# Optimization experiments

Hardware: AMD Instinct MI355X
Metric: run time of the kernel (lower is better)

The kernel has to match this reference:

```python
import jax, jax.numpy as jnp
import numpy as np

DIM = 128
B = 262144


def setup_inputs() -> dict:
    key = jax.random.key(0)
    k_t, k_w1, k_b1, k_w2, k_b2 = jax.random.split(key, 5)
    t = jax.random.uniform(k_t, (B,), dtype=jnp.float32)  # t in [0, 1]
    s = 1.0 / np.sqrt(DIM)  # torch Linear default init scale
    W1 = jax.random.uniform(k_w1, (DIM, DIM), dtype=jnp.float32, minval=-s, maxval=s)
    b1 = jax.random.uniform(k_b1, (DIM,), dtype=jnp.float32, minval=-s, maxval=s)
    W2 = jax.random.uniform(k_w2, (DIM, DIM), dtype=jnp.float32, minval=-s, maxval=s)
    b2 = jax.random.uniform(k_b2, (DIM,), dtype=jnp.float32, minval=-s, maxval=s)
    return {"t": t, "W1": W1, "b1": b1, "W2": W2, "b2": b2}


def reference(t, W1, b1, W2, b2):
    # create_timestep_embedding, vectorized over batch and dim:
    #   emb[b, i] = t[b]*cos(i/dim*pi*t[b]) + t[b]*sin(i/dim*pi*(1 - t[b]))
    phase = (jnp.arange(DIM, dtype=t.dtype) / DIM) * jnp.pi  # [DIM]
    tb = t[:, None]  # [B, 1]
    emb = tb * jnp.cos(phase[None, :] * tb) + tb * jnp.sin(phase[None, :] * (1.0 - tb))  # [B, DIM]
    x = jax.nn.silu(emb @ W1.T + b1)  # Linear128 + SiLU
    x = jax.nn.silu(x @ W2.T + b2)    # Linear128 + SiLU
    return x
```

## Files before the change

### kernel.cpp

```cpp
#include <hip/hip_runtime.h>

typedef _Float16 f16;
typedef _Float16 f16x2 __attribute__((ext_vector_type(2)));
typedef _Float16 f16x8 __attribute__((ext_vector_type(8)));
typedef float    f32x16 __attribute__((ext_vector_type(16)));

#define DIM 128

__device__ __forceinline__ float silu_f(float x) {
    float e = __builtin_amdgcn_exp2f(x * -1.44269504088896341f);
    return x * __builtin_amdgcn_rcpf(1.0f + e);
}

__global__ __launch_bounds__(512, 2)
void ts_mlp_kernel(const float* __restrict__ t,
                   const float* __restrict__ W1, const float* __restrict__ b1,
                   const float* __restrict__ W2, const float* __restrict__ b2,
                   float* __restrict__ out, int B) {
    __shared__ f16x8 w1f[8][4][64];
    __shared__ f16x8 w2f[8][4][64];
    __shared__ f16x2 x1p[8][512][4];

    const int tid  = threadIdx.x;
    const int wv   = tid >> 6;
    const int lane = tid & 63;
    const int h    = lane >> 5;
    const int l31  = lane & 31;
    const int par  = lane & 1;

    {
        const int kt = wv;
        const int k0 = kt * 16 + h * 8;
#pragma unroll
        for (int mtx = 0; mtx < 2; ++mtx) {
            const float* W = mtx ? W2 : W1;
#pragma unroll
            for (int nt = 0; nt < 4; ++nt) {
                const int n = nt * 32 + l31;
                const float4* src = (const float4*)(W + n * DIM + k0);
                float4 lo = src[0], hi = src[1];
                f16x8 fr;
                fr[0] = (f16)lo.x; fr[1] = (f16)lo.y; fr[2] = (f16)lo.z; fr[3] = (f16)lo.w;
                fr[4] = (f16)hi.x; fr[5] = (f16)hi.y; fr[6] = (f16)hi.z; fr[7] = (f16)hi.w;
                if (mtx) w2f[kt][nt][lane] = fr; else w1f[kt][nt][lane] = fr;
            }
        }
    }
    float b1v[4], b2v[4];
#pragma unroll
    for (int nt = 0; nt < 4; ++nt) {
        b1v[nt] = b1[nt * 32 + l31];
        b2v[nt] = b2[nt * 32 + l31];
    }
    __syncthreads();

    const int ntiles = B >> 8;
    int tile = blockIdx.x;
    float tv_next = (tile < ntiles) ? t[tile * 256 + wv * 32 + l31] : 0.0f;
    const float h8f = (float)(h * 8);

    for (; tile < ntiles; tile += gridDim.x) {
        const float tv = tv_next;
        const int nxt = tile + gridDim.x;
        if (nxt < ntiles) tv_next = t[nxt * 256 + wv * 32 + l31];
        const int row0 = tile * 256 + wv * 32;

        const float t256 = tv * 0.00390625f;
        const float o256 = (1.0f - tv) * 0.00390625f;
        f16x8 af[8];
#pragma unroll
        for (int kt = 0; kt < 8; ++kt) {
#pragma unroll
            for (int j = 0; j < 8; ++j) {
                const float fd = (float)(kt * 16 + j) + h8f;
                const float c  = __builtin_amdgcn_cosf(fd * t256);
                const float s  = __builtin_amdgcn_sinf(fd * o256);
                af[kt][j] = (f16)(tv * (c + s));
            }
        }

        f32x16 acc[4];
#pragma unroll
        for (int nt = 0; nt < 4; ++nt)
#pragma unroll
            for (int r = 0; r < 16; ++r) acc[nt][r] = 0.0f;
#pragma unroll
        for (int kt = 0; kt < 8; ++kt) {
#pragma unroll
            for (int nt = 0; nt < 4; ++nt) {
                acc[nt] = __builtin_amdgcn_mfma_f32_32x32x16_f16(
                    af[kt], w1f[kt][nt][lane], acc[nt], 0, 0, 0);
            }
        }

#pragma unroll
        for (int nt = 0; nt < 4; ++nt) {
            float v[16], pv[16];
#pragma unroll
            for (int r = 0; r < 16; ++r) v[r] = silu_f(acc[nt][r] + b1v[nt]);
#pragma unroll
            for (int r = 0; r < 16; ++r) pv[r] = __shfl_xor(v[r], 1, 64);
            const int cch = nt * 4 + ((lane & 30) >> 3);
            const int dw  = (lane & 6) >> 1;
#pragma unroll
            for (int w8 = 0; w8 < 8; ++w8) {
                const int r   = par * 8 + w8;
                const int row = (r & 3) + 8 * (r >> 2) + 4 * h;
                const float lo = par ? pv[r] : v[r];
                const float hi = par ? v[r] : pv[r];
                f16x2 hh; hh.x = (f16)lo; hh.y = (f16)hi;
                x1p[wv][row * 16 + (cch ^ (row & 15))][dw] = hh;
            }
        }

        f32x16 acc2[4];
#pragma unroll
        for (int nt = 0; nt < 4; ++nt)
#pragma unroll
            for (int r = 0; r < 16; ++r) acc2[nt][r] = 0.0f;
#pragma unroll
        for (int kt = 0; kt < 8; ++kt) {
            const f16x8 a2 = *(const f16x8*)&x1p[wv][l31 * 16 + ((kt * 2 + h) ^ (l31 & 15))][0];
#pragma unroll
            for (int nt = 0; nt < 4; ++nt) {
                acc2[nt] = __builtin_amdgcn_mfma_f32_32x32x16_f16(
                    a2, w2f[kt][nt][lane], acc2[nt], 0, 0, 0);
            }
        }

#pragma unroll
        for (int nt = 0; nt < 4; ++nt) {
#pragma unroll
            for (int r = 0; r < 16; ++r) {
                const int row = (r & 3) + 8 * (r >> 2) + 4 * h;
                const float o = silu_f(acc2[nt][r] + b2v[nt]);
                out[(size_t)(row0 + row) * DIM + nt * 32 + l31] = o;
            }
        }
    }
}

extern "C" void kernel_launch(void* const* d_in, const int* in_sizes, int n_in,
                              void* d_out, int out_size, void* d_ws, size_t ws_size,
                              hipStream_t stream) {
    const float* t  = (const float*)d_in[0];
    const float* W1 = (const float*)d_in[1];
    const float* b1 = (const float*)d_in[2];
    const float* W2 = (const float*)d_in[3];
    const float* b2 = (const float*)d_in[4];
    float* out = (float*)d_out;
    const int B = in_sizes[0];
    const int ntiles = B >> 8;
    int grid = ntiles < 256 ? ntiles : 256;
    ts_mlp_kernel<<<dim3(grid), dim3(512), 0, stream>>>(t, W1, b1, W2, b2, out, B);
}
```

Baseline: 194.6 us.

## Transpose MFMA operands to keep hidden activations in registers, drop LDS staging

The MFMA operands are swapped so the accumulator holds the transposed product, which lets the first layer's SiLU output be repacked into the second layer's B operand with cross-half lane shuffles instead of a round trip through shared memory. The embedding is now computed per k-tile inside the first GEMM loop, and the output is written as 16-byte vector stores per row. Dropping the LDS buffer frees shared memory, so occupancy is raised to 4 blocks per CU and the grid is doubled. Bias values are now read from global memory inside the epilogue, and the tighter launch bound may force register spills.

```diff
diff --git a/kernel.cpp b/kernel.cpp
--- a/kernel.cpp
+++ b/kernel.cpp
@@ -3,30 +3,31 @@
 typedef _Float16 f16;
 typedef _Float16 f16x2 __attribute__((ext_vector_type(2)));
 typedef _Float16 f16x8 __attribute__((ext_vector_type(8)));
+typedef float    f32x4 __attribute__((ext_vector_type(4)));
 typedef float    f32x16 __attribute__((ext_vector_type(16)));
 
 #define DIM 128
+
+union U8 { f16x8 v; unsigned int u[4]; };
 
 __device__ __forceinline__ float silu_f(float x) {
     float e = __builtin_amdgcn_exp2f(x * -1.44269504088896341f);
     return x * __builtin_amdgcn_rcpf(1.0f + e);
 }
 
-__global__ __launch_bounds__(512, 2)
+__global__ __launch_bounds__(512, 4)
 void ts_mlp_kernel(const float* __restrict__ t,
                    const float* __restrict__ W1, const float* __restrict__ b1,
                    const float* __restrict__ W2, const float* __restrict__ b2,
                    float* __restrict__ out, int B) {
     __shared__ f16x8 w1f[8][4][64];
     __shared__ f16x8 w2f[8][4][64];
-    __shared__ f16x2 x1p[8][512][4];
 
     const int tid  = threadIdx.x;
     const int wv   = tid >> 6;
     const int lane = tid & 63;
     const int h    = lane >> 5;
     const int l31  = lane & 31;
-    const int par  = lane & 1;
 
     {
         const int kt = wv;
@@ -46,39 +47,24 @@
             }
         }
     }
-    float b1v[4], b2v[4];
-#pragma unroll
-    for (int nt = 0; nt < 4; ++nt) {
-        b1v[nt] = b1[nt * 32 + l31];
-        b2v[nt] = b2[nt * 32 + l31];
-    }
     __syncthreads();
 
     const int ntiles = B >> 8;
+    const int stride = gridDim.x;
+    const float h8f = (float)(h * 8);
+
     int tile = blockIdx.x;
     float tv_next = (tile < ntiles) ? t[tile * 256 + wv * 32 + l31] : 0.0f;
-    const float h8f = (float)(h * 8);
 
-    for (; tile < ntiles; tile += gridDim.x) {
+#pragma unroll 1
+    for (; tile < ntiles; tile += stride) {
         const float tv = tv_next;
-        const int nxt = tile + gridDim.x;
+        const int nxt = tile + stride;
         if (nxt < ntiles) tv_next = t[nxt * 256 + wv * 32 + l31];
         const int row0 = tile * 256 + wv * 32;
 
         const float t256 = tv * 0.00390625f;
         const float o256 = (1.0f - tv) * 0.00390625f;
-        f16x8 af[8];
-#pragma unroll
-        for (int kt = 0; kt < 8; ++kt) {
-#pragma unroll
-            for (int j = 0; j < 8; ++j) {
-                const float fd = (float)(kt * 16 + j) + h8f;
-                const float c  = __builtin_amdgcn_cosf(fd * t256);
-                const float s  = __builtin_amdgcn_sinf(fd * o256);
-                af[kt][j] = (f16)(tv * (c + s));
-            }
-        }
-
         f32x16 acc[4];
 #pragma unroll
         for (int nt = 0; nt < 4; ++nt)
@@ -86,30 +72,47 @@
             for (int r = 0; r < 16; ++r) acc[nt][r] = 0.0f;
 #pragma unroll
         for (int kt = 0; kt < 8; ++kt) {
+            f16x8 ef;
+#pragma unroll
+            for (int j = 0; j < 8; ++j) {
+                const float fd = (float)(kt * 16 + j) + h8f;
+                const float c  = __builtin_amdgcn_cosf(fd * t256);
+                const float s  = __builtin_amdgcn_sinf(fd * o256);
+                ef[j] = (f16)(tv * (c + s));
+            }
 #pragma unroll
             for (int nt = 0; nt < 4; ++nt) {
                 acc[nt] = __builtin_amdgcn_mfma_f32_32x32x16_f16(
-                    af[kt], w1f[kt][nt][lane], acc[nt], 0, 0, 0);
+                    w1f[kt][nt][lane], ef, acc[nt], 0, 0, 0);
             }
         }
 
+        unsigned int K0[8], K1[8], R0[8], R1[8];
 #pragma unroll
         for (int nt = 0; nt < 4; ++nt) {
-            float v[16], pv[16];
+            unsigned int D[4][2];
 #pragma unroll
-            for (int r = 0; r < 16; ++r) v[r] = silu_f(acc[nt][r] + b1v[nt]);
+            for (int rr = 0; rr < 4; ++rr) {
 #pragma unroll
-            for (int r = 0; r < 16; ++r) pv[r] = __shfl_xor(v[r], 1, 64);
-            const int cch = nt * 4 + ((lane & 30) >> 3);
-            const int dw  = (lane & 6) >> 1;
+                for (int qp = 0; qp < 2; ++qp) {
+                    const int r  = 4 * rr + 2 * qp;
+                    const int nb = 32 * nt + 8 * rr + 2 * qp;
+                    const float z0 = acc[nt][r]     + (h ? b1[nb + 4] : b1[nb]);
+                    const float z1 = acc[nt][r + 1] + (h ? b1[nb + 5] : b1[nb + 1]);
+                    f16x2 p; p.x = (f16)silu_f(z0); p.y = (f16)silu_f(z1);
+                    D[rr][qp] = __builtin_bit_cast(unsigned int, p);
+                }
+            }
 #pragma unroll
-            for (int w8 = 0; w8 < 8; ++w8) {
-                const int r   = par * 8 + w8;
-                const int row = (r & 3) + 8 * (r >> 2) + 4 * h;
-                const float lo = par ? pv[r] : v[r];
-                const float hi = par ? v[r] : pv[r];
-                f16x2 hh; hh.x = (f16)lo; hh.y = (f16)hi;
-                x1p[wv][row * 16 + (cch ^ (row & 15))][dw] = hh;
+            for (int i = 0; i < 2; ++i) {
+                const unsigned int s0 = h ? D[2 * i][0] : D[2 * i + 1][0];
+                const unsigned int s1 = h ? D[2 * i][1] : D[2 * i + 1][1];
+                const unsigned int r0 = (unsigned int)__shfl_xor((int)s0, 32, 64);
+                const unsigned int r1 = (unsigned int)__shfl_xor((int)s1, 32, 64);
+                K0[2 * nt + i] = h ? D[2 * i + 1][0] : D[2 * i][0];
+                K1[2 * nt + i] = h ? D[2 * i + 1][1] : D[2 * i][1];
+                R0[2 * nt + i] = r0;
+                R1[2 * nt + i] = r1;
             }
         }
 
@@ -120,21 +123,31 @@
             for (int r = 0; r < 16; ++r) acc2[nt][r] = 0.0f;
 #pragma unroll
         for (int kt = 0; kt < 8; ++kt) {
-            const f16x8 a2 = *(const f16x8*)&x1p[wv][l31 * 16 + ((kt * 2 + h) ^ (l31 & 15))][0];
+            U8 bf;
+            bf.u[0] = h ? R0[kt] : K0[kt];
+            bf.u[1] = h ? R1[kt] : K1[kt];
+            bf.u[2] = h ? K0[kt] : R0[kt];
+            bf.u[3] = h ? K1[kt] : R1[kt];
 #pragma unroll
             for (int nt = 0; nt < 4; ++nt) {
                 acc2[nt] = __builtin_amdgcn_mfma_f32_32x32x16_f16(
-                    a2, w2f[kt][nt][lane], acc2[nt], 0, 0, 0);
+                    w2f[kt][nt][lane], bf.v, acc2[nt], 0, 0, 0);
             }
         }
 
+        const size_t rbase = (size_t)(row0 + l31) * DIM;
 #pragma unroll
         for (int nt = 0; nt < 4; ++nt) {
 #pragma unroll
-            for (int r = 0; r < 16; ++r) {
-                const int row = (r & 3) + 8 * (r >> 2) + 4 * h;
-                const float o = silu_f(acc2[nt][r] + b2v[nt]);
-                out[(size_t)(row0 + row) * DIM + nt * 32 + l31] = o;
+            for (int rr = 0; rr < 4; ++rr) {
+                f32x4 o;
+#pragma unroll
+                for (int q = 0; q < 4; ++q) {
+                    const int r  = 4 * rr + q;
+                    const int nb = 32 * nt + 8 * rr + q;
+                    o[q] = silu_f(acc2[nt][r] + (h ? b2[nb + 4] : b2[nb]));
+                }
+                *(f32x4*)&out[rbase + 32 * nt + 8 * rr + 4 * h] = o;
             }
         }
     }
@@ -151,6 +164,6 @@
     float* out = (float*)d_out;
     const int B = in_sizes[0];
     const int ntiles = B >> 8;
-    int grid = ntiles < 256 ? ntiles : 256;
+    int grid = ntiles < 512 ? ntiles : 512;
     ts_mlp_kernel<<<dim3(grid), dim3(512), 0, stream>>>(t, W1, b1, W2, b2, out, B);
 }
```

Measured after the change: 470.5 us. +141.8%, slower.
